# Kernel tuning notes

Hardware: AMD Instinct MI355X
Metric: run time of the kernel (lower is better)

Reference implementation:

```python
import jax, jax.numpy as jnp
import numpy as np

N = 50000      # nodes
E = 800000     # edges
FIN = 128      # num_feature
EDIM = 16      # edge_dim
OUT = 64       # out_dim (per-head channels; concat=False averages heads)
H = 4          # heads
SCALE = 1.0 / float(np.sqrt(OUT))


def _layernorm(h, g, b):
    mu = h.mean(-1, keepdims=True)
    var = ((h - mu) ** 2).mean(-1, keepdims=True)
    return (h - mu) * jax.lax.rsqrt(var + 1e-5) * g + b


def _tconv(x, src, dst, ea, Wq, bq, Wk, bk, Wv, bv, We, Ws, bs):
    # PyG TransformerConv, concat=False, root_weight=True, eval mode (no dropout)
    n = x.shape[0]
    q = (x @ Wq + bq).reshape(n, H, OUT)[dst]   # [E,H,D] query at destination
    k = (x @ Wk + bk).reshape(n, H, OUT)[src]   # [E,H,D] key at source
    v = (x @ Wv + bv).reshape(n, H, OUT)[src]   # [E,H,D] value at source
    e = (ea @ We).reshape(-1, H, OUT)           # [E,H,D] edge embedding (no bias)
    logits = jnp.einsum('ehd,ehd->eh', q, k + e) * SCALE   # [E,H]
    # segment softmax over incoming edges of each destination node
    m = jax.lax.stop_gradient(jax.ops.segment_max(logits, dst, num_segments=n))
    a = jnp.exp(logits - m[dst])
    s = jax.ops.segment_sum(a, dst, num_segments=n)
    alpha = a / s[dst]                                     # [E,H]
    agg = jax.ops.segment_sum((v + e) * alpha[..., None], dst, num_segments=n)  # [N,H,D]
    return agg.mean(axis=1) + x @ Ws + bs      # concat=False -> head mean; + skip


def _forward(x, src, dst, ea, p1, p2, p3, g, b):
    h = x
    for p in (p1, p2, p3):
        h = jax.nn.gelu(_layernorm(_tconv(h, src, dst, ea, *p), g, b), approximate=False)
    return h


def setup_inputs() -> dict:
    key = jax.random.key(0)
    ks = iter(jax.random.split(key, 64))
    def nrm(shp, s=0.05):
        return jax.random.normal(next(ks), shp, jnp.float32) * s
    inp = {
        'x': nrm((N, FIN), 1.0),
        'edge_index': jax.random.randint(next(ks), (2, E), 0, N),
        'edge_attr': nrm((E, EDIM), 1.0),
    }
    for l, fin in ((1, FIN), (2, OUT), (3, OUT)):
        inp[f'Wq{l}'] = nrm((fin, H * OUT)); inp[f'bq{l}'] = jnp.zeros((H * OUT,), jnp.float32)
        inp[f'Wk{l}'] = nrm((fin, H * OUT)); inp[f'bk{l}'] = jnp.zeros((H * OUT,), jnp.float32)
        inp[f'Wv{l}'] = nrm((fin, H * OUT)); inp[f'bv{l}'] = jnp.zeros((H * OUT,), jnp.float32)
        inp[f'We{l}'] = nrm((EDIM, H * OUT))
        inp[f'Ws{l}'] = nrm((fin, OUT)); inp[f'bs{l}'] = jnp.zeros((OUT,), jnp.float32)
    inp['ln_g'] = jnp.ones((OUT,), jnp.float32)
    inp['ln_b'] = jnp.zeros((OUT,), jnp.float32)
    return inp


def reference(x, edge_index, edge_attr,
              Wq1, bq1, Wk1, bk1, Wv1, bv1, We1, Ws1, bs1,
              Wq2, bq2, Wk2, bk2, Wv2, bv2, We2, Ws2, bs2,
              Wq3, bq3, Wk3, bk3, Wv3, bv3, We3, Ws3, bs3,
              ln_g, ln_b):
    src, dst = edge_index[0], edge_index[1]
    p1 = (Wq1, bq1, Wk1, bk1, Wv1, bv1, We1, Ws1, bs1)
    p2 = (Wq2, bq2, Wk2, bk2, Wv2, bv2, We2, Ws2, bs2)
    p3 = (Wq3, bq3, Wk3, bk3, Wv3, bv3, We3, Ws3, bs3)
    return _forward(x, src, dst, edge_attr, p1, p2, p3, ln_g, ln_b)
```

## Files before the change

kernel.cpp:

```cpp
#include <hip/hip_runtime.h>
#include <hip/hip_bf16.h>
#include <math.h>

#define NNODES 50000
#define NEDGES 800000
#define HD     256
#define CW     384
#define NTOT   896
#define QS     0.18033688011112042f

typedef __hip_bfloat16 bf16;
typedef unsigned short u16;
typedef unsigned char  u8;
typedef unsigned int   u32;
typedef unsigned long long u64;
typedef __attribute__((ext_vector_type(8))) short bf16x8;
typedef __attribute__((ext_vector_type(4))) float f32x4;
typedef __attribute__((ext_vector_type(2))) float f32x2;

__device__ __forceinline__ float lo16f(u32 u) { return __uint_as_float(u << 16); }
__device__ __forceinline__ float hi16f(u32 u) { return __uint_as_float(u & 0xFFFF0000u); }
__device__ __forceinline__ short f2s(float v) { __hip_bfloat16 h = __float2bfloat16(v); return *(short*)&h; }

template<int CTRL>
__device__ __forceinline__ float dppadd(float x) {
    int t = __builtin_amdgcn_update_dpp(0, __float_as_int(x), CTRL, 0xF, 0xF, true);
    return x + __int_as_float(t);
}

__global__ void hist_kernel(const int* __restrict__ dst, int* __restrict__ deg, int E) {
    int e = blockIdx.x * 256 + threadIdx.x;
    if (e < E) atomicAdd(&deg[dst[e]], 1);
}

__global__ void scanA(const int* __restrict__ deg, int* __restrict__ locincl,
                      int* __restrict__ blocksum, int n) {
    int tid = threadIdx.x;
    int i = blockIdx.x * 256 + tid;
    int v = (i < n) ? deg[i] : 0;
    int lane = tid & 63, w = tid >> 6;
    int s = v;
    #pragma unroll
    for (int off = 1; off < 64; off <<= 1) {
        int t = __shfl_up(s, off);
        if (lane >= off) s += t;
    }
    __shared__ int wsum[4];
    if (lane == 63) wsum[w] = s;
    __syncthreads();
    for (int ww = 0; ww < w; ww++) s += wsum[ww];
    if (i < n) locincl[i] = s;
    if (tid == 255) blocksum[blockIdx.x] = s;
}

__global__ void scanB(const int* __restrict__ blocksum, int* __restrict__ blockoff,
                      int nb, int* __restrict__ rowptr, int n) {
    int tid = threadIdx.x;
    int v = (tid < nb) ? blocksum[tid] : 0;
    int lane = tid & 63, w = tid >> 6;
    int s = v;
    #pragma unroll
    for (int off = 1; off < 64; off <<= 1) {
        int t = __shfl_up(s, off);
        if (lane >= off) s += t;
    }
    __shared__ int wsum[4];
    if (lane == 63) wsum[w] = s;
    __syncthreads();
    for (int ww = 0; ww < w; ww++) s += wsum[ww];
    if (tid < nb) blockoff[tid] = s - v;
    if (tid == 255) rowptr[n] = s;
}

__global__ void scanC(const int* __restrict__ deg, const int* __restrict__ locincl,
                      const int* __restrict__ blockoff,
                      int* __restrict__ rowptr, int* __restrict__ cursor, int n) {
    int i = blockIdx.x * 256 + threadIdx.x;
    if (i < n) {
        int ex = locincl[i] - deg[i] + blockoff[blockIdx.x];
        rowptr[i] = ex;
        cursor[i] = ex;
    }
}

__global__ void scatter_kernel(const int* __restrict__ src, const int* __restrict__ dst,
                               int* __restrict__ cursor, int2* __restrict__ csr2, int E) {
    int e = blockIdx.x * 256 + threadIdx.x;
    if (e < E) {
        int d = dst[e];
        int p = atomicAdd(&cursor[d], 1);
        csr2[p] = make_int2(src[e], e);
    }
}

__global__ void pack_all(const float* __restrict__ Wq, const float* __restrict__ bq,
                         const float* __restrict__ Wk, const float* __restrict__ bk,
                         const float* __restrict__ Wv, const float* __restrict__ bv,
                         const float* __restrict__ We,
                         const float* __restrict__ Ws, const float* __restrict__ bs,
                         bf16* __restrict__ Wc, float* __restrict__ b, int K) {
    int n = blockIdx.x, c = threadIdx.x;
    float v, bb;
    if (n < 256)      { v = Wq[(size_t)c * 256 + n] * QS;    bb = bq[n] * QS; }
    else if (n < 320) {
        int t = n - 256, h = t >> 4, j = t & 15;
        float s = 0.f, sb = 0.f;
        #pragma unroll 8
        for (int d = 0; d < 64; d++) {
            float wv = We[j * HD + h * 64 + d];
            s += Wq[(size_t)c * 256 + h * 64 + d] * wv;
            sb += bq[h * 64 + d] * wv;
        }
        v = s * QS; bb = sb * QS;
    }
    else if (n < 384) { v = Ws[(size_t)c * 64  + (n - 320)]; bb = bs[n - 320]; }
    else if (n < 640) { v = Wv[(size_t)c * 256 + (n - 384)]; bb = bv[n - 384]; }
    else              { v = Wk[(size_t)c * 256 + (n - 640)]; bb = bk[n - 640]; }
    Wc[(size_t)n * K + c] = __float2bfloat16(v);
    if (c == 0) b[n] = bb;
}

template<typename TA, int K>
__global__ void __launch_bounds__(256) gemm_fused(
    const TA* __restrict__ A, const bf16* __restrict__ Wc, const float* __restrict__ bias,
    bf16* __restrict__ comb, bf16* __restrict__ vbuf, u8* __restrict__ k8)
{
    constexpr int KS = K / 32;
    int tid = threadIdx.x, w = tid >> 6, lane = tid & 63;
    int cl = lane & 15, aq = lane >> 4;
    int m = blockIdx.x * 64 + w * 16 + cl;
    int rowc = (m < NNODES) ? m : (NNODES - 1);
    int cbeg = blockIdx.y * 7;

    bf16x8 af[KS];
    if constexpr (sizeof(TA) == 4) {
        const float* ar = (const float*)A + (size_t)rowc * K;
        #pragma unroll
        for (int ks = 0; ks < KS; ks++) {
            const float4* ap = (const float4*)(ar + ks * 32 + aq * 8);
            float4 f0 = ap[0], f1 = ap[1];
            union { short s[8]; bf16x8 v; } t;
            t.s[0] = f2s(f0.x); t.s[1] = f2s(f0.y); t.s[2] = f2s(f0.z); t.s[3] = f2s(f0.w);
            t.s[4] = f2s(f1.x); t.s[5] = f2s(f1.y); t.s[6] = f2s(f1.z); t.s[7] = f2s(f1.w);
            af[ks] = t.v;
        }
    } else {
        const u16* ar = (const u16*)A + (size_t)rowc * K;
        #pragma unroll
        for (int ks = 0; ks < KS; ks++) af[ks] = *(const bf16x8*)(ar + ks * 32 + aq * 8);
    }

    for (int ci = 0; ci < 7; ci++) {
        int chunk = cbeg + ci;
        const u16* wbase = (const u16*)Wc + (size_t)chunk * 64 * K + (size_t)cl * K + aq * 8;
        f32x4 acc[4] = {};
        #pragma unroll
        for (int t = 0; t < 4; t++) {
            #pragma unroll
            for (int ks = 0; ks < KS; ks++) {
                bf16x8 bfr = *(const bf16x8*)(wbase + (size_t)t * 16 * K + ks * 32);
                acc[t] = __builtin_amdgcn_mfma_f32_16x16x32_bf16(bfr, af[ks], acc[t], 0, 0, 0);
            }
        }
        if (m >= NNODES) continue;
        if (chunk < 10) {
            u16* dst;
            if (chunk < 6) dst = (u16*)comb + (size_t)m * CW + chunk * 64;
            else           dst = (u16*)vbuf + (size_t)m * 256 + (chunk - 6) * 64;
            #pragma unroll
            for (int t = 0; t < 4; t++) {
                float4 bv = *(const float4*)&bias[chunk * 64 + t * 16 + aq * 4];
                u32 lo = (u32)(u16)f2s(acc[t][0] + bv.x) | ((u32)(u16)f2s(acc[t][1] + bv.y) << 16);
                u32 hi = (u32)(u16)f2s(acc[t][2] + bv.z) | ((u32)(u16)f2s(acc[t][3] + bv.w) << 16);
                *(uint2*)(dst + t * 16 + aq * 4) = make_uint2(lo, hi);
            }
        } else {
            u8* dst = k8 + (size_t)m * 256 + (chunk - 10) * 64;
            #pragma unroll
            for (int t = 0; t < 4; t++) {
                float4 bv = *(const float4*)&bias[chunk * 64 + t * 16 + aq * 4];
                u32 pk = __builtin_amdgcn_cvt_pk_fp8_f32(acc[t][0] + bv.x, acc[t][1] + bv.y, 0, false);
                pk = __builtin_amdgcn_cvt_pk_fp8_f32(acc[t][2] + bv.z, acc[t][3] + bv.w, pk, true);
                *(u32*)(dst + t * 16 + aq * 4) = pk;
            }
        }
    }
}

__global__ void __launch_bounds__(256) node_fused(
    const int* __restrict__ rowptr, const int2* __restrict__ csr2,
    const float* __restrict__ eattr, const u16* __restrict__ comb,
    const u16* __restrict__ vbuf, const u8* __restrict__ k8,
    const float* __restrict__ We, const float* __restrict__ lng, const float* __restrict__ lnb,
    bf16* __restrict__ outB, float* __restrict__ outF)
{
    int tid = threadIdx.x, w = tid >> 6, lane = tid & 63;
    int n = blockIdx.x * 4 + w;
    int hg = lane >> 4, j16 = lane & 15, coff = 4 * lane;
    __shared__ float sAV[4][256];
    __shared__ float sAE[4][64];

    const u16* crow = comb + (size_t)n * CW;
    uint2 qv = *(const uint2*)(crow + coff);
    float qf0 = lo16f(qv.x), qf1 = hi16f(qv.x), qf2 = lo16f(qv.y), qf3 = hi16f(qv.y);
    float qwe_r = __uint_as_float((u32)crow[256 + lane] << 16);

    int e0 = __builtin_amdgcn_readfirstlane(rowptr[n]);
    int e1 = __builtin_amdgcn_readfirstlane(rowptr[n + 1]);

    float ss = 0.f, av0 = 0.f, av1 = 0.f, av2 = 0.f, av3 = 0.f, ae = 0.f;
    u32 vo = (u32)coff * 2u;
    u32 eo = (u32)j16 * 4u;

    auto EDGE = [&](int2 me) {
        u32 s   = (u32)__builtin_amdgcn_readfirstlane(me.x);
        u32 eid = (u32)__builtin_amdgcn_readfirstlane(me.y);
        const char* kp = (const char*)k8    + ((size_t)s << 8);
        const char* vp = (const char*)vbuf  + ((size_t)s << 9);
        const char* ep = (const char*)eattr + ((size_t)eid << 6);
        u32   kw = *(const u32*)  (kp + coff);
        uint2 vw = *(const uint2*)(vp + vo);
        float ea = *(const float*)(ep + eo);
        f32x2 k01 = __builtin_amdgcn_cvt_pk_f32_fp8(kw, false);
        f32x2 k23 = __builtin_amdgcn_cvt_pk_f32_fp8(kw, true);
        float part = qf0 * k01[0] + qf1 * k01[1] + qf2 * k23[0] + qf3 * k23[1] + qwe_r * ea;
        part = dppadd<0xB1>(part);
        part = dppadd<0x4E>(part);
        part = dppadd<0x141>(part);
        part = dppadd<0x140>(part);
        float alpha = __builtin_amdgcn_exp2f(part);
        ss += alpha;
        ae += alpha * ea;
        av0 += alpha * lo16f(vw.x); av1 += alpha * hi16f(vw.x);
        av2 += alpha * lo16f(vw.y); av3 += alpha * hi16f(vw.y);
    };

    int i = e0;
    int2 c0 = make_int2(0, 0), c1 = c0, c2 = c0, c3 = c0;
    if (i + 3 < e1) { c0 = csr2[i]; c1 = csr2[i + 1]; c2 = csr2[i + 2]; c3 = csr2[i + 3]; }
    for (; i + 7 < e1; i += 4) {
        int2 p0 = csr2[i + 4], p1 = csr2[i + 5], p2 = csr2[i + 6], p3 = csr2[i + 7];
        EDGE(c0); EDGE(c1); EDGE(c2); EDGE(c3);
        c0 = p0; c1 = p1; c2 = p2; c3 = p3;
    }
    if (i + 3 < e1) { EDGE(c0); EDGE(c1); EDGE(c2); EDGE(c3); i += 4; }
    for (; i < e1; ++i) { int2 cc = csr2[i]; EDGE(cc); }

    float inv = (ss > 0.f) ? 1.f / ss : 0.f;
    *(float4*)&sAV[w][coff] = make_float4(av0 * inv, av1 * inv, av2 * inv, av3 * inv);
    sAE[w][lane] = ae * inv;

    int d = lane;
    float val = 0.f;
    #pragma unroll
    for (int h = 0; h < 4; h++) {
        float xv = sAV[w][h * 64 + d];
        #pragma unroll
        for (int j = 0; j < 16; j++) xv += sAE[w][h * 16 + j] * We[j * HD + h * 64 + d];
        val += xv;
    }
    val = val * 0.25f + __uint_as_float((u32)crow[320 + d] << 16);

    float m = val;
    #pragma unroll
    for (int off = 1; off < 64; off <<= 1) m += __shfl_xor(m, off);
    m *= (1.f / 64.f);
    float diff = val - m;
    float vr = diff * diff;
    #pragma unroll
    for (int off = 1; off < 64; off <<= 1) vr += __shfl_xor(vr, off);
    vr *= (1.f / 64.f);
    float y = diff * rsqrtf(vr + 1e-5f) * lng[d] + lnb[d];
    float ge = 0.5f * y * (1.f + erff(y * 0.70710678118654752f));
    if (outF) outF[(size_t)n * 64 + d] = ge;
    else      outB[(size_t)n * 64 + d] = __float2bfloat16(ge);
}

extern "C" void kernel_launch(void* const* d_in, const int* in_sizes, int n_in,
                              void* d_out, int out_size, void* d_ws, size_t ws_size,
                              hipStream_t stream)
{
    const float* x     = (const float*)d_in[0];
    const int*   eidx  = (const int*)d_in[1];
    const float* eattr = (const float*)d_in[2];
    struct P { const float *Wq,*bq,*Wk,*bk,*Wv,*bv,*We,*Ws,*bs; };
    P p[3];
    for (int l = 0; l < 3; l++) {
        int base = 3 + l * 9;
        p[l].Wq = (const float*)d_in[base + 0]; p[l].bq = (const float*)d_in[base + 1];
        p[l].Wk = (const float*)d_in[base + 2]; p[l].bk = (const float*)d_in[base + 3];
        p[l].Wv = (const float*)d_in[base + 4]; p[l].bv = (const float*)d_in[base + 5];
        p[l].We = (const float*)d_in[base + 6];
        p[l].Ws = (const float*)d_in[base + 7]; p[l].bs = (const float*)d_in[base + 8];
    }
    const float* lng = (const float*)d_in[30];
    const float* lnb = (const float*)d_in[31];

    char* ws = (char*)d_ws;
    size_t off = 0;
    auto alloc = [&](size_t bytes) { void* pp = ws + off; off += (bytes + 255) & ~(size_t)255; return pp; };
    int*   rowptr   = (int*)  alloc((NNODES + 1) * 4);
    int*   cursor   = (int*)  alloc(NNODES * 4);
    int*   deg      = (int*)  alloc(NNODES * 4);
    int*   blocksum = (int*)  alloc(256 * 4);
    int*   blockoff = (int*)  alloc(256 * 4);
    int2*  csr2     = (int2*) alloc((size_t)NEDGES * 8);
    bf16*  hbuf     = (bf16*) alloc((size_t)NNODES * 64 * 2);
    bf16*  comb     = (bf16*) alloc((size_t)NNODES * CW * 2);
    bf16*  vbuf     = (bf16*) alloc((size_t)NNODES * 256 * 2);
    u8*    k8       = (u8*)   alloc((size_t)NNODES * 256);
    bf16*  Wc       = (bf16*) alloc((size_t)NTOT * 128 * 2);
    float* b896     = (float*)alloc(NTOT * 4);
    (void)ws_size;

    const int* srcArr = eidx;
    const int* dstArr = eidx + NEDGES;

    int NB = (NNODES + 255) / 256;
    (void)hipMemsetAsync(deg, 0, NNODES * 4, stream);
    hist_kernel<<<(NEDGES + 255) / 256, 256, 0, stream>>>(dstArr, deg, NEDGES);
    scanA<<<NB, 256, 0, stream>>>(deg, cursor, blocksum, NNODES);
    scanB<<<1, 256, 0, stream>>>(blocksum, blockoff, NB, rowptr, NNODES);
    scanC<<<NB, 256, 0, stream>>>(deg, cursor, blockoff, rowptr, cursor, NNODES);
    scatter_kernel<<<(NEDGES + 255) / 256, 256, 0, stream>>>(srcArr, dstArr, cursor, csr2, NEDGES);

    int gm = (NNODES + 63) / 64;
    int fins[3] = {128, 64, 64};

    const void* hin = x;
    for (int l = 0; l < 3; l++) {
        int FIN = fins[l];
        pack_all<<<NTOT, FIN, 0, stream>>>(p[l].Wq, p[l].bq, p[l].Wk, p[l].bk,
                                           p[l].Wv, p[l].bv, p[l].We, p[l].Ws, p[l].bs,
                                           Wc, b896, FIN);
        if (l == 0) gemm_fused<float, 128><<<dim3(gm, 2), 256, 0, stream>>>((const float*)hin, Wc, b896, comb, vbuf, k8);
        else        gemm_fused<bf16,  64><<<dim3(gm, 2), 256, 0, stream>>>((const bf16*)hin,  Wc, b896, comb, vbuf, k8);
        node_fused<<<NNODES / 4, 256, 0, stream>>>(rowptr, csr2, eattr, (const u16*)comb,
            (const u16*)vbuf, k8, p[l].We, lng, lnb,
            (l == 2) ? nullptr : hbuf, (l == 2) ? (float*)d_out : nullptr);
        hin = hbuf;
    }
}
```

Baseline: 788.3 us.

## Stage weight tiles in swizzled LDS and loop blocks over multiple row tiles

The projection GEMM now loads a 128-column slice of packed weights into XOR-swizzled shared memory once per block. Each block then walks four 64-row tiles of node features, prefetching the next A tile into registers while issuing MFMAs against the LDS-resident weights. Previously every wave streamed weight fragments from global memory for each of 7 column chunks. The grid changes from (rows, 2) to (7 column pairs, row groups), which raises LDS use and register pressure per block.

```diff
diff --git a/kernel.cpp b/kernel.cpp
--- a/kernel.cpp
+++ b/kernel.cpp
@@ -121,69 +121,93 @@
 }
 
 template<typename TA, int K>
-__global__ void __launch_bounds__(256) gemm_fused(
+__global__ void __launch_bounds__(256) gemm_lds(
     const TA* __restrict__ A, const bf16* __restrict__ Wc, const float* __restrict__ bias,
     bf16* __restrict__ comb, bf16* __restrict__ vbuf, u8* __restrict__ k8)
 {
-    constexpr int KS = K / 32;
+    constexpr int KS  = K / 32;
+    constexpr int CPR = K / 8;
+    constexpr int ITERS = 4;
+    __shared__ short Bl[128 * K];
     int tid = threadIdx.x, w = tid >> 6, lane = tid & 63;
     int cl = lane & 15, aq = lane >> 4;
-    int m = blockIdx.x * 64 + w * 16 + cl;
-    int rowc = (m < NNODES) ? m : (NNODES - 1);
-    int cbeg = blockIdx.y * 7;
-
-    bf16x8 af[KS];
-    if constexpr (sizeof(TA) == 4) {
-        const float* ar = (const float*)A + (size_t)rowc * K;
-        #pragma unroll
-        for (int ks = 0; ks < KS; ks++) {
-            const float4* ap = (const float4*)(ar + ks * 32 + aq * 8);
-            float4 f0 = ap[0], f1 = ap[1];
-            union { short s[8]; bf16x8 v; } t;
-            t.s[0] = f2s(f0.x); t.s[1] = f2s(f0.y); t.s[2] = f2s(f0.z); t.s[3] = f2s(f0.w);
-            t.s[4] = f2s(f1.x); t.s[5] = f2s(f1.y); t.s[6] = f2s(f1.z); t.s[7] = f2s(f1.w);
-            af[ks] = t.v;
-        }
-    } else {
-        const u16* ar = (const u16*)A + (size_t)rowc * K;
-        #pragma unroll
-        for (int ks = 0; ks < KS; ks++) af[ks] = *(const bf16x8*)(ar + ks * 32 + aq * 8);
-    }
-
-    for (int ci = 0; ci < 7; ci++) {
-        int chunk = cbeg + ci;
-        const u16* wbase = (const u16*)Wc + (size_t)chunk * 64 * K + (size_t)cl * K + aq * 8;
-        f32x4 acc[4] = {};
-        #pragma unroll
-        for (int t = 0; t < 4; t++) {
+    int c0 = blockIdx.x * 2;
+
+    #pragma unroll
+    for (int p = 0; p < CPR / 2; p++) {
+        int slot = tid + p * 256;
+        int row = slot / CPR, j = slot % CPR;
+        *(uint4*)&Bl[row * K + ((j ^ (row & 7)) << 3)] =
+            *(const uint4*)((const u16*)Wc + (size_t)(c0 * 64 + row) * K + (j << 3));
+    }
+    __syncthreads();
+
+    int mrow = blockIdx.y * (64 * ITERS) + w * 16 + cl;
+
+    auto LOADA = [&](bf16x8* af, int m) {
+        int rc = (m < NNODES) ? m : (NNODES - 1);
+        if constexpr (sizeof(TA) == 4) {
+            const float* ar = (const float*)A + (size_t)rc * K + aq * 8;
             #pragma unroll
             for (int ks = 0; ks < KS; ks++) {
-                bf16x8 bfr = *(const bf16x8*)(wbase + (size_t)t * 16 * K + ks * 32);
-                acc[t] = __builtin_amdgcn_mfma_f32_16x16x32_bf16(bfr, af[ks], acc[t], 0, 0, 0);
+                const float4* ap = (const float4*)(ar + ks * 32);
+                float4 f0 = ap[0], f1 = ap[1];
+                union { short s[8]; bf16x8 v; } t;
+                t.s[0] = f2s(f0.x); t.s[1] = f2s(f0.y); t.s[2] = f2s(f0.z); t.s[3] = f2s(f0.w);
+                t.s[4] = f2s(f1.x); t.s[5] = f2s(f1.y); t.s[6] = f2s(f1.z); t.s[7] = f2s(f1.w);
+                af[ks] = t.v;
+            }
+        } else {
+            const u16* ar = (const u16*)A + (size_t)rc * K + aq * 8;
+            #pragma unroll
+            for (int ks = 0; ks < KS; ks++) af[ks] = *(const bf16x8*)(ar + ks * 32);
+        }
+    };
+
+    bf16x8 cur[KS], nxt[KS];
+    LOADA(cur, mrow);
+    #pragma unroll
+    for (int it = 0; it < ITERS; it++) {
+        int m = mrow + it * 64;
+        if (it + 1 < ITERS) LOADA(nxt, m + 64);
+        #pragma unroll
+        for (int c = 0; c < 2; c++) {
+            int chunk = c0 + c;
+            f32x4 acc[4] = {};
+            #pragma unroll
+            for (int t = 0; t < 4; t++) {
+                #pragma unroll
+                for (int ks = 0; ks < KS; ks++) {
+                    bf16x8 bfr = *(const bf16x8*)&Bl[(c * 64 + t * 16 + cl) * K +
+                                                     (((ks * 4 + aq) ^ (cl & 7)) << 3)];
+                    acc[t] = __builtin_amdgcn_mfma_f32_16x16x32_bf16(bfr, cur[ks], acc[t], 0, 0, 0);
+                }
+            }
+            if (m < NNODES) {
+                if (chunk < 10) {
+                    u16* dst = (chunk < 6) ? (u16*)comb + (size_t)m * CW + chunk * 64
+                                           : (u16*)vbuf + (size_t)m * 256 + (chunk - 6) * 64;
+                    #pragma unroll
+                    for (int t = 0; t < 4; t++) {
+                        float4 bv = *(const float4*)&bias[chunk * 64 + t * 16 + aq * 4];
+                        u32 lo = (u32)(u16)f2s(acc[t][0] + bv.x) | ((u32)(u16)f2s(acc[t][1] + bv.y) << 16);
+                        u32 hi = (u32)(u16)f2s(acc[t][2] + bv.z) | ((u32)(u16)f2s(acc[t][3] + bv.w) << 16);
+                        *(uint2*)(dst + t * 16 + aq * 4) = make_uint2(lo, hi);
+                    }
+                } else {
+                    u8* dst = k8 + (size_t)m * 256 + (chunk - 10) * 64;
+                    #pragma unroll
+                    for (int t = 0; t < 4; t++) {
+                        float4 bv = *(const float4*)&bias[chunk * 64 + t * 16 + aq * 4];
+                        u32 pk = __builtin_amdgcn_cvt_pk_fp8_f32(acc[t][0] + bv.x, acc[t][1] + bv.y, 0, false);
+                        pk = __builtin_amdgcn_cvt_pk_fp8_f32(acc[t][2] + bv.z, acc[t][3] + bv.w, pk, true);
+                        *(u32*)(dst + t * 16 + aq * 4) = pk;
+                    }
+                }
             }
         }
-        if (m >= NNODES) continue;
-        if (chunk < 10) {
-            u16* dst;
-            if (chunk < 6) dst = (u16*)comb + (size_t)m * CW + chunk * 64;
-            else           dst = (u16*)vbuf + (size_t)m * 256 + (chunk - 6) * 64;
-            #pragma unroll
-            for (int t = 0; t < 4; t++) {
-                float4 bv = *(const float4*)&bias[chunk * 64 + t * 16 + aq * 4];
-                u32 lo = (u32)(u16)f2s(acc[t][0] + bv.x) | ((u32)(u16)f2s(acc[t][1] + bv.y) << 16);
-                u32 hi = (u32)(u16)f2s(acc[t][2] + bv.z) | ((u32)(u16)f2s(acc[t][3] + bv.w) << 16);
-                *(uint2*)(dst + t * 16 + aq * 4) = make_uint2(lo, hi);
-            }
-        } else {
-            u8* dst = k8 + (size_t)m * 256 + (chunk - 10) * 64;
-            #pragma unroll
-            for (int t = 0; t < 4; t++) {
-                float4 bv = *(const float4*)&bias[chunk * 64 + t * 16 + aq * 4];
-                u32 pk = __builtin_amdgcn_cvt_pk_fp8_f32(acc[t][0] + bv.x, acc[t][1] + bv.y, 0, false);
-                pk = __builtin_amdgcn_cvt_pk_fp8_f32(acc[t][2] + bv.z, acc[t][3] + bv.w, pk, true);
-                *(u32*)(dst + t * 16 + aq * 4) = pk;
-            }
-        }
+        #pragma unroll
+        for (int ks = 0; ks < KS; ks++) cur[ks] = nxt[ks];
     }
 }
 
@@ -324,7 +348,7 @@
     scanC<<<NB, 256, 0, stream>>>(deg, cursor, blockoff, rowptr, cursor, NNODES);
     scatter_kernel<<<(NEDGES + 255) / 256, 256, 0, stream>>>(srcArr, dstArr, cursor, csr2, NEDGES);
 
-    int gm = (NNODES + 63) / 64;
+    int NBY = (NNODES + 255) / 256;
     int fins[3] = {128, 64, 64};
 
     const void* hin = x;
@@ -333,8 +357,8 @@
         pack_all<<<NTOT, FIN, 0, stream>>>(p[l].Wq, p[l].bq, p[l].Wk, p[l].bk,
                                            p[l].Wv, p[l].bv, p[l].We, p[l].Ws, p[l].bs,
                                            Wc, b896, FIN);
-        if (l == 0) gemm_fused<float, 128><<<dim3(gm, 2), 256, 0, stream>>>((const float*)hin, Wc, b896, comb, vbuf, k8);
-        else        gemm_fused<bf16,  64><<<dim3(gm, 2), 256, 0, stream>>>((const bf16*)hin,  Wc, b896, comb, vbuf, k8);
+        if (l == 0) gemm_lds<float, 128><<<dim3(7, NBY), 256, 0, stream>>>((const float*)hin, Wc, b896, comb, vbuf, k8);
+        else        gemm_lds<bf16,  64><<<dim3(7, NBY), 256, 0, stream>>>((const bf16*)hin,  Wc, b896, comb, vbuf, k8);
         node_fused<<<NNODES / 4, 256, 0, stream>>>(rowptr, csr2, eattr, (const u16*)comb,
             (const u16*)vbuf, k8, p[l].We, lng, lnb,
             (l == 2) ? nullptr : hbuf, (l == 2) ? (float*)d_out : nullptr);
```

After: 689.9 us. -12.5%, faster.
